# Kernel tuning notes

Measured on AMD Instinct MI355X. Metric: run time of the kernel, lower is better.

The kernel has to match this reference:

```python
import jax, jax.numpy as jnp
import numpy as np

MAX_SPAN_LEN = 6

def setup_inputs() -> dict:
    key = jax.random.key(0)
    k1, k2 = jax.random.split(key)
    B, L, H = 16, 1024, 768
    span_adjacency = jax.random.uniform(k1, (B, L, L, 1), dtype=jnp.float32)
    bound_hidden = jax.random.normal(k2, (B, L, H), dtype=jnp.float32)
    return {"span_adjacency": span_adjacency, "bound_hidden": bound_hidden}

def reference(span_adjacency, bound_hidden):
    # out[:, j] = sum_{i=j}^{min(j+6,L)-1} w[:,j,i] * concat(h[:,i], h[:,j])
    B, L, H = bound_hidden.shape
    d = jnp.arange(MAX_SPAN_LEN)                      # window offsets [6]
    j = jnp.arange(L)                                  # [L]
    idx = jnp.minimum(j[:, None] + d[None, :], L - 1)  # [L, 6] clamped gather index
    valid = (j[:, None] + d[None, :]) < L              # [L, 6] window mask
    # gather window weights: w[:, j, j+d] -> [B, L, 6]
    w = span_adjacency[:, j[:, None], idx, 0] * valid.astype(span_adjacency.dtype)
    # gather window hiddens: h[:, j+d] -> [B, L, 6, H]
    h_win = bound_hidden[:, idx]
    first = jnp.einsum('bjd,bjdh->bjh', w, h_win)      # sum_i w * h_i
    wsum = jnp.sum(w, axis=-1, keepdims=True)          # [B, L, 1]
    second = bound_hidden * wsum                       # h_j * sum_i w
    return jnp.concatenate([first, second], axis=-1)   # [B, L, 2H]
```

## Files before the change

### kernel.cpp

```cpp
#include <hip/hip_runtime.h>
#include <hip/hip_bf16.h>


#define LROWS 1024
#define HDIM  768
#define SPANW 6
#define VEC_PER_ROW (HDIM / 4)

__global__ __launch_bounds__(256) void boundary_seg_kernel(
    const float* __restrict__ span,
    const float* __restrict__ bound,
    float* __restrict__ out)
{
    const int v  = blockIdx.x * 256 + threadIdx.x;
    const int hv = v % VEC_PER_ROW;
    const int t  = v / VEC_PER_ROW;
    const int j  = t & (LROWS - 1);
    const int bL = t - j;

    const float* srow = span + (size_t)t * LROWS + j;
    float w[SPANW];
    float wsum = 0.f;
#pragma unroll
    for (int d = 0; d < SPANW; ++d) {
        float wd = 0.f;
        if (j + d < LROWS) wd = srow[d];
        w[d] = wd;
        wsum += wd;
    }

    float4 acc = make_float4(0.f, 0.f, 0.f, 0.f);
    float4 h0;
#pragma unroll
    for (int d = 0; d < SPANW; ++d) {
        int row = j + d;
        if (row > LROWS - 1) row = LROWS - 1;
        const float4 h =
            *(const float4*)(bound + (size_t)(bL + row) * HDIM + hv * 4);
        if (d == 0) h0 = h;
        acc.x += w[d] * h.x;
        acc.y += w[d] * h.y;
        acc.z += w[d] * h.z;
        acc.w += w[d] * h.w;
    }

    const float4 sec = make_float4(h0.x * wsum, h0.y * wsum,
                                   h0.z * wsum, h0.w * wsum);

    float* orow = out + (size_t)t * (2 * HDIM) + hv * 4;
    *(float4*)(orow)        = acc;
    *(float4*)(orow + HDIM) = sec;
}

extern "C" void kernel_launch(void* const* d_in, const int* in_sizes, int n_in,
                              void* d_out, int out_size, void* d_ws, size_t ws_size,
                              hipStream_t stream) {
    const float* span  = (const float*)d_in[0];
    const float* bound = (const float*)d_in[1];
    float* out = (float*)d_out;

    const int B = in_sizes[1] / (LROWS * HDIM);
    const int total_vecs = B * LROWS * VEC_PER_ROW;
    dim3 grid(total_vecs / 256), block(256);
    hipLaunchKernelGGL(boundary_seg_kernel, grid, block, 0, stream,
                       span, bound, out);
}
```

Baseline: 183.1 us.

## Stage sliding window of hidden rows in LDS per 8-row tile

Each block now handles 8 consecutive output rows of one batch. It loads the 13 needed hidden rows and the window weights into shared memory once, then computes every output from LDS. Before, each thread fetched its 6 hidden vectors from global memory, which caused about 6x redundant reads. Outputs are written with nontemporal stores to avoid polluting the cache. The trade-offs are about 40KB of LDS per block, which limits occupancy, and a sync barrier between the load phase and the compute phase.

```diff
diff --git a/kernel.cpp b/kernel.cpp
--- a/kernel.cpp
+++ b/kernel.cpp
@@ -5,51 +5,71 @@
 #define LROWS 1024
 #define HDIM  768
 #define SPANW 6
+#define TILE_J 8
+#define STAGE (TILE_J + SPANW - 1)
 #define VEC_PER_ROW (HDIM / 4)
+#define WPT (TILE_J * VEC_PER_ROW / 256)
+
+typedef float f32x4 __attribute__((ext_vector_type(4)));
 
 __global__ __launch_bounds__(256) void boundary_seg_kernel(
     const float* __restrict__ span,
     const float* __restrict__ bound,
     float* __restrict__ out)
 {
-    const int v  = blockIdx.x * 256 + threadIdx.x;
-    const int hv = v % VEC_PER_ROW;
-    const int t  = v / VEC_PER_ROW;
-    const int j  = t & (LROWS - 1);
-    const int bL = t - j;
+    __shared__ float sb[STAGE * HDIM];
+    __shared__ float sw[TILE_J][SPANW];
+    __shared__ float swsum[TILE_J];
 
-    const float* srow = span + (size_t)t * LROWS + j;
-    float w[SPANW];
-    float wsum = 0.f;
-#pragma unroll
-    for (int d = 0; d < SPANW; ++d) {
-        float wd = 0.f;
-        if (j + d < LROWS) wd = srow[d];
-        w[d] = wd;
-        wsum += wd;
+    const int tid = threadIdx.x;
+    const int b   = blockIdx.x >> 7;
+    const int j0  = (blockIdx.x & 127) * TILE_J;
+    const int bL  = b * LROWS;
+
+    f32x4* sb4 = (f32x4*)sb;
+    for (int i = tid; i < STAGE * VEC_PER_ROW; i += 256) {
+        const int s  = i / VEC_PER_ROW;
+        const int hv = i % VEC_PER_ROW;
+        int gr = j0 + s;
+        if (gr > LROWS - 1) gr = LROWS - 1;
+        sb4[i] = *(const f32x4*)(bound + (size_t)(bL + gr) * HDIM + hv * 4);
     }
 
-    float4 acc = make_float4(0.f, 0.f, 0.f, 0.f);
-    float4 h0;
+    if (tid < TILE_J) {
+        const int j = j0 + tid;
+        const float* srow = span + (size_t)(bL + j) * LROWS + j;
+        float wsum = 0.f;
 #pragma unroll
-    for (int d = 0; d < SPANW; ++d) {
-        int row = j + d;
-        if (row > LROWS - 1) row = LROWS - 1;
-        const float4 h =
-            *(const float4*)(bound + (size_t)(bL + row) * HDIM + hv * 4);
-        if (d == 0) h0 = h;
-        acc.x += w[d] * h.x;
-        acc.y += w[d] * h.y;
-        acc.z += w[d] * h.z;
-        acc.w += w[d] * h.w;
+        for (int d = 0; d < SPANW; ++d) {
+            float wd = (j + d < LROWS) ? srow[d] : 0.f;
+            sw[tid][d] = wd;
+            wsum += wd;
+        }
+        swsum[tid] = wsum;
     }
+    __syncthreads();
 
-    const float4 sec = make_float4(h0.x * wsum, h0.y * wsum,
-                                   h0.z * wsum, h0.w * wsum);
+#pragma unroll
+    for (int k = 0; k < WPT; ++k) {
+        const int item = tid + k * 256;
+        const int jj   = item / VEC_PER_ROW;
+        const int hv   = item % VEC_PER_ROW;
 
-    float* orow = out + (size_t)t * (2 * HDIM) + hv * 4;
-    *(float4*)(orow)        = acc;
-    *(float4*)(orow + HDIM) = sec;
+        f32x4 acc = (f32x4)(0.f);
+        f32x4 h0;
+#pragma unroll
+        for (int d = 0; d < SPANW; ++d) {
+            const float wd = sw[jj][d];
+            const f32x4 h = sb4[(jj + d) * VEC_PER_ROW + hv];
+            if (d == 0) h0 = h;
+            acc += wd * h;
+        }
+        const f32x4 sec = h0 * swsum[jj];
+
+        float* orow = out + (size_t)(bL + j0 + jj) * (2 * HDIM) + hv * 4;
+        __builtin_nontemporal_store(acc, (f32x4*)orow);
+        __builtin_nontemporal_store(sec, (f32x4*)(orow + HDIM));
+    }
 }
 
 extern "C" void kernel_launch(void* const* d_in, const int* in_sizes, int n_in,
@@ -60,8 +80,7 @@
     float* out = (float*)d_out;
 
     const int B = in_sizes[1] / (LROWS * HDIM);
-    const int total_vecs = B * LROWS * VEC_PER_ROW;
-    dim3 grid(total_vecs / 256), block(256);
+    dim3 grid(B * (LROWS / TILE_J)), block(256);
     hipLaunchKernelGGL(boundary_seg_kernel, grid, block, 0, stream,
                        span, bound, out);
 }
```

After: 182.9 us. Within noise of the previous version (-0.1%).
